# Optimization experiments

Measured on AMD Instinct MI355X. Metric: run time of the kernel, lower is better.

Reference implementation:

```python
import jax, jax.numpy as jnp
import numpy as np

D_MODEL = 1024
N_HEADS = 16
D_HEAD = 64
D_MLP = 4096
EPS = 1e-6


def setup_inputs() -> dict:
    key = jax.random.key(0)
    ks = jax.random.split(key, 12)
    s = lambda fan_in: 1.0 / np.sqrt(fan_in)
    x = jax.random.normal(ks[0], (2, 2048, D_MODEL), dtype=jnp.float32)
    inp = {
        "x": x,
        "ln1_w": jnp.ones((D_MODEL,), jnp.float32),
        "ln2_w": jnp.ones((D_MODEL,), jnp.float32),
        "Wq": jax.random.normal(ks[1], (D_MODEL, N_HEADS * D_HEAD), jnp.float32) * s(D_MODEL),
        "bq": jnp.zeros((N_HEADS * D_HEAD,), jnp.float32),
        "Wk": jax.random.normal(ks[2], (D_MODEL, N_HEADS * D_HEAD), jnp.float32) * s(D_MODEL),
        "bk": jnp.zeros((N_HEADS * D_HEAD,), jnp.float32),
        "Wv": jax.random.normal(ks[3], (D_MODEL, N_HEADS * D_HEAD), jnp.float32) * s(D_MODEL),
        "bv": jnp.zeros((N_HEADS * D_HEAD,), jnp.float32),
        "Wo": jax.random.normal(ks[4], (N_HEADS * D_HEAD, D_MODEL), jnp.float32) * s(N_HEADS * D_HEAD),
        "bo": jnp.zeros((D_MODEL,), jnp.float32),
        "Wup": jax.random.normal(ks[5], (D_MODEL, D_MLP), jnp.float32) * s(D_MODEL),
        "bup": jnp.zeros((D_MLP,), jnp.float32),
        "Wdown": jax.random.normal(ks[6], (D_MLP, D_MODEL), jnp.float32) * s(D_MLP),
        "bdown": jnp.zeros((D_MODEL,), jnp.float32),
    }
    return inp


def _rmsnorm(x, w):
    xf = x.astype(jnp.float32)
    norm = jax.lax.rsqrt(jnp.mean(xf * xf, axis=-1, keepdims=True) + EPS)
    return (x * norm).astype(x.dtype) * w


def _attention(x, Wq, bq, Wk, bk, Wv, bv, Wo, bo):
    B, T, _ = x.shape
    q = (x @ Wq + bq).reshape(B, T, N_HEADS, D_HEAD)
    k = (x @ Wk + bk).reshape(B, T, N_HEADS, D_HEAD)
    v = (x @ Wv + bv).reshape(B, T, N_HEADS, D_HEAD)
    # [B, H, Tq, Tk]
    attn = jnp.einsum("bqhd,bkhd->bhqk", q, k) / jnp.sqrt(jnp.float32(D_HEAD))
    causal = jnp.tril(jnp.ones((T, T), dtype=bool))
    attn = jnp.where(causal, attn, -jnp.inf)
    attn = jax.nn.softmax(attn, axis=-1)
    out = jnp.einsum("bhqk,bkhd->bqhd", attn, v).reshape(B, T, N_HEADS * D_HEAD)
    return out @ Wo + bo


def reference(x, ln1_w, ln2_w, Wq, bq, Wk, bk, Wv, bv, Wo, bo, Wup, bup, Wdown, bdown):
    x = x + _attention(_rmsnorm(x, ln1_w), Wq, bq, Wk, bk, Wv, bv, Wo, bo)
    h = _rmsnorm(x, ln2_w)
    mlp = jax.nn.gelu(h @ Wup + bup, approximate=False) @ Wdown + bdown
    return x + mlp
```

## Files before the change

kernel.cpp:

```cpp
#include <hip/hip_runtime.h>
#include <cmath>

#define DM   1024
#define HDS  16
#define DH   64
#define DMLP 4096
#define TSEQ 2048
#define NROW 4096

typedef short bf16x8 __attribute__((ext_vector_type(8)));
typedef float f32x4 __attribute__((ext_vector_type(4)));

__device__ __forceinline__ unsigned short f2bf(float f) {
  union { float f; unsigned u; } v; v.f = f;
  unsigned r = v.u + 0x7fffu + ((v.u >> 16) & 1u);
  return (unsigned short)(r >> 16);
}

__device__ __forceinline__ void gload_lds16(const void* g, void* l) {
  __builtin_amdgcn_global_load_lds(
      (const __attribute__((address_space(1))) unsigned int*)g,
      (__attribute__((address_space(3))) unsigned int*)l, 16, 0, 0);
}

__global__ __launch_bounds__(256) void tr_kernel(const float* __restrict__ in,
                                                 unsigned short* __restrict__ out,
                                                 int K, int N) {
  __shared__ unsigned short tile[32][33];
  int n0 = blockIdx.x * 32, k0 = blockIdx.y * 32;
  int tx = threadIdx.x & 31, ty = threadIdx.x >> 5;
#pragma unroll
  for (int j = 0; j < 4; ++j) {
    int k = ty + j * 8;
    tile[k][tx] = f2bf(in[(size_t)(k0 + k) * N + n0 + tx]);
  }
  __syncthreads();
#pragma unroll
  for (int j = 0; j < 4; ++j) {
    int n = ty + j * 8;
    out[(size_t)(n0 + n) * K + k0 + tx] = tile[tx][n];
  }
}

__global__ void concat3_kernel(const float* __restrict__ a, const float* __restrict__ b,
                               const float* __restrict__ c, float* __restrict__ out, int n) {
  int i = blockIdx.x * 256 + threadIdx.x;
  if (i < n) { out[i] = a[i]; out[n + i] = b[i]; out[2 * n + i] = c[i]; }
}

__global__ __launch_bounds__(256) void rmsnorm_kernel(const float* __restrict__ x,
                                                      const float* __restrict__ w,
                                                      unsigned short* __restrict__ out) {
  int row = blockIdx.x;
  int t = threadIdx.x;
  const float4* xr = (const float4*)(x + (size_t)row * DM);
  float4 v = xr[t];
  float ss = v.x * v.x + v.y * v.y + v.z * v.z + v.w * v.w;
#pragma unroll
  for (int m = 1; m < 64; m <<= 1) ss += __shfl_xor(ss, m, 64);
  __shared__ float sred[4];
  if ((t & 63) == 0) sred[t >> 6] = ss;
  __syncthreads();
  ss = sred[0] + sred[1] + sred[2] + sred[3];
  float norm = rsqrtf(ss * (1.0f / DM) + 1e-6f);
  float4 wv = ((const float4*)w)[t];
  ushort4 o;
  o.x = f2bf(v.x * norm * wv.x);
  o.y = f2bf(v.y * norm * wv.y);
  o.z = f2bf(v.z * norm * wv.z);
  o.w = f2bf(v.w * norm * wv.w);
  ((ushort4*)out)[(size_t)row * (DM / 4) + t] = o;
}

template <int EPI>
__global__ __launch_bounds__(256) void gemm_bt(const unsigned short* __restrict__ A,
                                               const unsigned short* __restrict__ BT,
                                               const float* __restrict__ bias,
                                               const float* __restrict__ res,
                                               void* __restrict__ outp,
                                               int M, int N, int K) {
  __shared__ alignas(16) unsigned short As[2][128 * 32];
  __shared__ alignas(16) unsigned short Bs[2][128 * 32];
  int tid = threadIdx.x;
  int w = tid >> 6, l = tid & 63;
  unsigned nx = gridDim.x;
  unsigned bidl = blockIdx.y * nx + blockIdx.x;
  unsigned nwg = nx * gridDim.y;
  unsigned cpx = nwg >> 3;
  unsigned sb = (bidl & 7) * cpx + (bidl >> 3);
  int m0 = (int)(sb / nx) * 128, n0 = (int)(sb % nx) * 128;
  int wr = w >> 1, wc = w & 1;
  f32x4 acc[4][4];
#pragma unroll
  for (int i = 0; i < 4; ++i)
#pragma unroll
    for (int j = 0; j < 4; ++j)
#pragma unroll
      for (int e = 0; e < 4; ++e) acc[i][j][e] = 0.0f;

  int nk = K >> 5;
  int arow = tid >> 2, aslot = tid & 3;

#define STG128(BUF, KT)                                                            \
  {                                                                                \
    _Pragma("unroll") for (int i = 0; i < 2; ++i) {                                \
      int row = i * 64 + arow;                                                     \
      gload_lds16(A + (size_t)(m0 + row) * K + (size_t)(KT) * 32 + aslot * 8,      \
                  (char*)As[BUF] + i * 4096 + w * 1024);                           \
      gload_lds16(BT + (size_t)(n0 + row) * K + (size_t)(KT) * 32 + aslot * 8,     \
                  (char*)Bs[BUF] + i * 4096 + w * 1024);                           \
    }                                                                              \
  }

  STG128(0, 0);
  __syncthreads();
  int cur = 0;
  for (int kt = 0; kt < nk; ++kt) {
    if (kt + 1 < nk) STG128(cur ^ 1, kt + 1);
    bf16x8 af[4], bfr[4];
#pragma unroll
    for (int mt = 0; mt < 4; ++mt)
      af[mt] = *(const bf16x8*)((const char*)As[cur] +
                (size_t)(wr * 64 + mt * 16 + (l & 15)) * 64 + (l >> 4) * 16);
#pragma unroll
    for (int nt = 0; nt < 4; ++nt)
      bfr[nt] = *(const bf16x8*)((const char*)Bs[cur] +
                 (size_t)(wc * 64 + nt * 16 + (l & 15)) * 64 + (l >> 4) * 16);
#pragma unroll
    for (int mt = 0; mt < 4; ++mt)
#pragma unroll
      for (int nt = 0; nt < 4; ++nt)
        acc[mt][nt] = __builtin_amdgcn_mfma_f32_16x16x32_bf16(af[mt], bfr[nt], acc[mt][nt], 0, 0, 0);
    __syncthreads();
    cur ^= 1;
  }
#undef STG128

  int g = l >> 4, c = l & 15;
#pragma unroll
  for (int mt = 0; mt < 4; ++mt) {
#pragma unroll
    for (int nt = 0; nt < 4; ++nt) {
#pragma unroll
      for (int r = 0; r < 4; ++r) {
        int m = m0 + wr * 64 + mt * 16 + g * 4 + r;
        int n = n0 + wc * 64 + nt * 16 + c;
        float v = acc[mt][nt][r] + bias[n];
        if (EPI == 2) v = 0.5f * v * (1.0f + erff(v * 0.70710678118654752f));
        if (EPI == 1) {
          v += res[(size_t)m * N + n];
          ((float*)outp)[(size_t)m * N + n] = v;
        } else {
          ((unsigned short*)outp)[(size_t)m * N + n] = f2bf(v);
        }
      }
    }
  }
}

template <int EPI>
__global__ __launch_bounds__(512) void gemm_db256(const unsigned short* __restrict__ A,
                                                  const unsigned short* __restrict__ BT,
                                                  const float* __restrict__ bias,
                                                  const float* __restrict__ res,
                                                  void* __restrict__ outp,
                                                  int M, int N, int K) {
  __shared__ alignas(16) unsigned short As[2][256 * 64];
  __shared__ alignas(16) unsigned short Bs[2][256 * 64];
  int tid = threadIdx.x;
  int w = tid >> 6, l = tid & 63;
  int wr = w >> 2, wc = w & 3;
  unsigned nx = gridDim.x;
  unsigned bidl = blockIdx.y * nx + blockIdx.x;
  unsigned nwg = nx * gridDim.y;
  unsigned cpx = nwg >> 3;
  unsigned sb = (bidl & 7) * cpx + (bidl >> 3);
  int m0 = (int)(sb / nx) * 256, n0 = (int)(sb % nx) * 256;

  f32x4 acc[8][4];
#pragma unroll
  for (int i = 0; i < 8; ++i)
#pragma unroll
    for (int j = 0; j < 4; ++j)
#pragma unroll
      for (int e = 0; e < 4; ++e) acc[i][j][e] = 0.0f;

  int nk = K >> 6;
  int srow = tid >> 3, sslot = tid & 7;
  int gslot = sslot ^ (srow & 7);
  int c = l & 15, g = l >> 4;

#define STG256(BUF, KT)                                                            \
  {                                                                                \
    _Pragma("unroll") for (int i = 0; i < 4; ++i) {                                \
      int row = i * 64 + srow;                                                     \
      gload_lds16(A + (size_t)(m0 + row) * K + (size_t)(KT) * 64 + gslot * 8,      \
                  (char*)As[BUF] + i * 8192 + w * 1024);                           \
      gload_lds16(BT + (size_t)(n0 + row) * K + (size_t)(KT) * 64 + gslot * 8,     \
                  (char*)Bs[BUF] + i * 8192 + w * 1024);                           \
    }                                                                              \
  }

  STG256(0, 0);
  __syncthreads();
  int cur = 0;
  for (int kt = 0; kt < nk; ++kt) {
    if (kt + 1 < nk) STG256(cur ^ 1, kt + 1);
#pragma unroll
    for (int ks = 0; ks < 2; ++ks) {
      bf16x8 bfr[4];
#pragma unroll
      for (int nt = 0; nt < 4; ++nt) {
        int brow = wc * 64 + nt * 16 + c;
        unsigned bslot = (unsigned)((ks * 4 + g) ^ (brow & 7));
        bfr[nt] = *(const bf16x8*)((const char*)Bs[cur] + (size_t)brow * 128 + bslot * 16);
      }
#pragma unroll
      for (int mt = 0; mt < 8; ++mt) {
        int arow2 = wr * 128 + mt * 16 + c;
        unsigned aslot2 = (unsigned)((ks * 4 + g) ^ (arow2 & 7));
        bf16x8 af = *(const bf16x8*)((const char*)As[cur] + (size_t)arow2 * 128 + aslot2 * 16);
#pragma unroll
        for (int nt = 0; nt < 4; ++nt)
          acc[mt][nt] = __builtin_amdgcn_mfma_f32_16x16x32_bf16(af, bfr[nt], acc[mt][nt], 0, 0, 0);
      }
    }
    __syncthreads();
    cur ^= 1;
  }
#undef STG256

#pragma unroll
  for (int mt = 0; mt < 8; ++mt) {
#pragma unroll
    for (int nt = 0; nt < 4; ++nt) {
#pragma unroll
      for (int r = 0; r < 4; ++r) {
        int m = m0 + wr * 128 + mt * 16 + g * 4 + r;
        int n = n0 + wc * 64 + nt * 16 + c;
        float v = acc[mt][nt][r] + bias[n];
        if (EPI == 2) v = 0.5f * v * (1.0f + erff(v * 0.70710678118654752f));
        if (EPI == 1) {
          v += res[(size_t)m * N + n];
          ((float*)outp)[(size_t)m * N + n] = v;
        } else {
          ((unsigned short*)outp)[(size_t)m * N + n] = f2bf(v);
        }
      }
    }
  }
}

__global__ __launch_bounds__(256) void vtr_kernel(const unsigned short* __restrict__ qkv,
                                                  unsigned short* __restrict__ vt) {
  __shared__ unsigned short tile[64][72];
  int bh = blockIdx.y, t0 = blockIdx.x * 64;
  int b = bh >> 4, h = bh & 15;
  int r = threadIdx.x >> 3, sl = threadIdx.x & 7;
#pragma unroll
  for (int half = 0; half < 2; ++half) {
    int rr = r + half * 32;
    bf16x8 v = *(const bf16x8*)(qkv + (size_t)(b * TSEQ + t0 + rr) * 3072 + 2048 + h * 64 + sl * 8);
    *(bf16x8*)&tile[rr][sl * 8] = v;
  }
  __syncthreads();
#pragma unroll
  for (int half = 0; half < 2; ++half) {
    int d = r + half * 32;
    bf16x8 o;
#pragma unroll
    for (int j = 0; j < 8; ++j) o[j] = (short)tile[sl * 8 + j][d];
    *(bf16x8*)(vt + ((size_t)bh * 64 + d) * TSEQ + t0 + sl * 8) = o;
  }
}

__global__ __launch_bounds__(256) void attn_kernel(const unsigned short* __restrict__ qkv,
                                                   const unsigned short* __restrict__ vt,
                                                   unsigned short* __restrict__ attn_out) {
  __shared__ alignas(16) unsigned short Ks[2][64 * 64];
  __shared__ alignas(16) unsigned short Vs[2][64 * 64];
  __shared__ alignas(16) unsigned short Ps[4][16 * 64];
  int tid = threadIdx.x, w = tid >> 6, l = tid & 63, g = l >> 4, c = l & 15;
  int bid = blockIdx.x;
  int qb = 31 - (bid & 31);
  int bh = bid >> 5, b = bh >> 4, h = bh & 15;
  int q0 = qb * 64;
  int qw = q0 + w * 16;

  bf16x8 qf[2];
#pragma unroll
  for (int s = 0; s < 2; ++s)
    qf[s] = *(const bf16x8*)(qkv + (size_t)(b * TSEQ + qw + c) * 3072 + h * 64 + s * 32 + g * 8);

  f32x4 o[4];
  float mrow[4], lpart[4];
#pragma unroll
  for (int dc = 0; dc < 4; ++dc)
#pragma unroll
    for (int e = 0; e < 4; ++e) o[dc][e] = 0.0f;
#pragma unroll
  for (int r = 0; r < 4; ++r) { mrow[r] = -1e30f; lpart[r] = 0.0f; }

  int ntile = qb + 1;
  int sr = tid >> 3, ss = tid & 7;
  bf16x8 kreg[2], vreg[2];

#define LOADT(K0)                                                                       \
  {                                                                                     \
    _Pragma("unroll") for (int hf = 0; hf < 2; ++hf) {                                  \
      int rr = sr + hf * 32;                                                            \
      kreg[hf] = *(const bf16x8*)(qkv + (size_t)(b * TSEQ + (K0) + rr) * 3072 + 1024 +  \
                                  h * 64 + ss * 8);                                     \
      vreg[hf] = *(const bf16x8*)(vt + ((size_t)bh * 64 + rr) * TSEQ + (K0) + ss * 8);  \
    }                                                                                   \
  }
#define WRITET(BUF)                                                                     \
  {                                                                                     \
    _Pragma("unroll") for (int hf = 0; hf < 2; ++hf) {                                  \
      int rr = sr + hf * 32;                                                            \
      unsigned off = (unsigned)(rr * 128 + ss * 16) ^ (unsigned)((rr & 7) << 4);        \
      *(bf16x8*)((char*)Ks[BUF] + off) = kreg[hf];                                      \
      *(bf16x8*)((char*)Vs[BUF] + off) = vreg[hf];                                      \
    }                                                                                   \
  }

  LOADT(0);
  WRITET(0);
  __syncthreads();

  for (int t = 0; t < ntile; ++t) {
    int k0 = t << 6, cur = t & 1;
    if (t + 1 < ntile) LOADT((t + 1) << 6);

    {
      const char* Kb = (const char*)Ks[cur];
      const char* Vb = (const char*)Vs[cur];
      f32x4 s[4];
#pragma unroll
      for (int ni = 0; ni < 4; ++ni) {
        int krow = ni * 16 + c;
        unsigned swz = (unsigned)((c & 7) << 4);
        bf16x8 kf0 = *(const bf16x8*)(Kb + (((unsigned)(krow * 128) + g * 16) ^ swz));
        bf16x8 kf1 = *(const bf16x8*)(Kb + (((unsigned)(krow * 128) + 64 + g * 16) ^ swz));
        f32x4 acc;
#pragma unroll
        for (int e = 0; e < 4; ++e) acc[e] = 0.0f;
        acc = __builtin_amdgcn_mfma_f32_16x16x32_bf16(qf[0], kf0, acc, 0, 0, 0);
        acc = __builtin_amdgcn_mfma_f32_16x16x32_bf16(qf[1], kf1, acc, 0, 0, 0);
        s[ni] = acc;
      }
      bool full = (k0 + 63 <= qw);
#pragma unroll
      for (int r = 0; r < 4; ++r) {
        int qg = qw + g * 4 + r;
        float pm[4];
#pragma unroll
        for (int ni = 0; ni < 4; ++ni) {
          float v = s[ni][r] * 0.125f;
          if (!full) {
            int kg = k0 + ni * 16 + c;
            v = (kg <= qg) ? v : -1e30f;
          }
          pm[ni] = v;
        }
        float mx = fmaxf(fmaxf(pm[0], pm[1]), fmaxf(pm[2], pm[3]));
        mx = fmaxf(mx, __shfl_xor(mx, 1, 64));
        mx = fmaxf(mx, __shfl_xor(mx, 2, 64));
        mx = fmaxf(mx, __shfl_xor(mx, 4, 64));
        mx = fmaxf(mx, __shfl_xor(mx, 8, 64));
        float mnew = fmaxf(mrow[r], mx);
        float scale = __expf(mrow[r] - mnew);
        mrow[r] = mnew;
        float p[4], rs = 0.0f;
#pragma unroll
        for (int ni = 0; ni < 4; ++ni) { p[ni] = __expf(pm[ni] - mnew); rs += p[ni]; }
        lpart[r] = lpart[r] * scale + rs;
#pragma unroll
        for (int dc = 0; dc < 4; ++dc) o[dc][r] *= scale;
        int prow = g * 4 + r;
        unsigned pswz = (unsigned)((prow & 7) << 4);
#pragma unroll
        for (int ni = 0; ni < 4; ++ni)
          *(unsigned short*)((char*)Ps[w] +
                             (((unsigned)(prow * 128 + (ni * 16 + c) * 2)) ^ pswz)) = f2bf(p[ni]);
      }
      asm volatile("s_waitcnt lgkmcnt(0)" ::: "memory");
      unsigned swz = (unsigned)((c & 7) << 4);
#pragma unroll
      for (int kc = 0; kc < 2; ++kc) {
        bf16x8 pf = *(const bf16x8*)((const char*)Ps[w] +
                     (((unsigned)(c * 128 + kc * 64 + g * 16)) ^ swz));
#pragma unroll
        for (int dc = 0; dc < 4; ++dc) {
          bf16x8 vf = *(const bf16x8*)(Vb +
                       (((unsigned)((dc * 16 + c) * 128 + kc * 64 + g * 16)) ^ swz));
          o[dc] = __builtin_amdgcn_mfma_f32_16x16x32_bf16(pf, vf, o[dc], 0, 0, 0);
        }
      }
    }

    if (t + 1 < ntile) {
      WRITET(cur ^ 1);
      __syncthreads();
    }
  }

#pragma unroll
  for (int r = 0; r < 4; ++r) {
    float lr = lpart[r];
    lr += __shfl_xor(lr, 1, 64);
    lr += __shfl_xor(lr, 2, 64);
    lr += __shfl_xor(lr, 4, 64);
    lr += __shfl_xor(lr, 8, 64);
    float inv = 1.0f / lr;
    size_t row = (size_t)b * TSEQ + qw + g * 4 + r;
    unsigned short* op = attn_out + row * 1024 + h * 64 + c;
#pragma unroll
    for (int dc = 0; dc < 4; ++dc) op[dc * 16] = f2bf(o[dc][r] * inv);
  }
#undef LOADT
#undef WRITET
}

extern "C" void kernel_launch(void* const* d_in, const int* in_sizes, int n_in,
                              void* d_out, int out_size, void* d_ws, size_t ws_size,
                              hipStream_t stream) {
  const float* x    = (const float*)d_in[0];
  const float* ln1w = (const float*)d_in[1];
  const float* ln2w = (const float*)d_in[2];
  const float* Wq   = (const float*)d_in[3];
  const float* bq   = (const float*)d_in[4];
  const float* Wk   = (const float*)d_in[5];
  const float* bk   = (const float*)d_in[6];
  const float* Wv   = (const float*)d_in[7];
  const float* bv   = (const float*)d_in[8];
  const float* Wo   = (const float*)d_in[9];
  const float* bo   = (const float*)d_in[10];
  const float* Wup  = (const float*)d_in[11];
  const float* bup  = (const float*)d_in[12];
  const float* Wdn  = (const float*)d_in[13];
  const float* bdn  = (const float*)d_in[14];

  char* ws = (char*)d_ws;
  unsigned short* xn1   = (unsigned short*)(ws + 0);
  unsigned short* vtb   = (unsigned short*)(ws + 0);
  unsigned short* qkv   = (unsigned short*)(ws + (8ull << 20));
  unsigned short* gbuf  = (unsigned short*)(ws + 0);
  unsigned short* attn  = (unsigned short*)(ws + (32ull << 20));
  float*          x2    = (float*)(ws + (40ull << 20));
  unsigned short* h2    = (unsigned short*)(ws + (56ull << 20));
  unsigned short* WqkvT = (unsigned short*)(ws + (64ull << 20));
  unsigned short* WoT   = (unsigned short*)(ws + (70ull << 20));
  unsigned short* WupT  = (unsigned short*)(ws + (72ull << 20));
  unsigned short* WdnT  = (unsigned short*)(ws + (80ull << 20));
  float*          bqkv  = (float*)(ws + (88ull << 20));

  dim3 blk(256);
  dim3 blk512(512);
  tr_kernel<<<dim3(32, 32), blk, 0, stream>>>(Wq, WqkvT, 1024, 1024);
  tr_kernel<<<dim3(32, 32), blk, 0, stream>>>(Wk, WqkvT + 1024 * 1024, 1024, 1024);
  tr_kernel<<<dim3(32, 32), blk, 0, stream>>>(Wv, WqkvT + 2 * 1024 * 1024, 1024, 1024);
  tr_kernel<<<dim3(32, 32), blk, 0, stream>>>(Wo, WoT, 1024, 1024);
  tr_kernel<<<dim3(128, 32), blk, 0, stream>>>(Wup, WupT, 1024, 4096);
  tr_kernel<<<dim3(32, 128), blk, 0, stream>>>(Wdn, WdnT, 4096, 1024);
  concat3_kernel<<<dim3(4), blk, 0, stream>>>(bq, bk, bv, bqkv, 1024);

  rmsnorm_kernel<<<dim3(NROW), blk, 0, stream>>>(x, ln1w, xn1);
  gemm_db256<0><<<dim3(12, 16), blk512, 0, stream>>>(xn1, WqkvT, bqkv, nullptr, qkv, NROW, 3072, 1024);

  vtr_kernel<<<dim3(32, 32), blk, 0, stream>>>(qkv, vtb);
  attn_kernel<<<dim3(1024), blk, 0, stream>>>(qkv, vtb, attn);

  gemm_bt<1><<<dim3(8, 32), blk, 0, stream>>>(attn, WoT, bo, x, x2, NROW, 1024, 1024);

  rmsnorm_kernel<<<dim3(NROW), blk, 0, stream>>>(x2, ln2w, h2);
  gemm_db256<2><<<dim3(16, 16), blk512, 0, stream>>>(h2, WupT, bup, nullptr, gbuf, NROW, 4096, 1024);
  gemm_bt<1><<<dim3(8, 32), blk, 0, stream>>>(gbuf, WdnT, bdn, x2, d_out, NROW, 1024, 4096);
}
```

Measured before the change: 472.7 us.

## Pair causal query blocks per workgroup to balance load and share K/V tiles

Each attention workgroup now handles two query blocks, a high one (31-p) and a low one (p), so every workgroup processes 33 key tiles in total. Each K/V tile loaded into LDS is reused by both query blocks, and the grid drops from 1024 to 512 workgroups. This balances the triangular causal workload and cuts K/V reloads. The cost is twice the accumulator registers per thread, which may lower occupancy, plus fewer workgroups to spread across the CUs.

```diff
diff --git a/kernel.cpp b/kernel.cpp
--- a/kernel.cpp
+++ b/kernel.cpp
@@ -279,29 +279,32 @@
                                                    unsigned short* __restrict__ attn_out) {
   __shared__ alignas(16) unsigned short Ks[2][64 * 64];
   __shared__ alignas(16) unsigned short Vs[2][64 * 64];
-  __shared__ alignas(16) unsigned short Ps[4][16 * 64];
+  __shared__ alignas(16) unsigned short Ps[4][2][16 * 64];
   int tid = threadIdx.x, w = tid >> 6, l = tid & 63, g = l >> 4, c = l & 15;
   int bid = blockIdx.x;
-  int qb = 31 - (bid & 31);
-  int bh = bid >> 5, b = bh >> 4, h = bh & 15;
-  int q0 = qb * 64;
-  int qw = q0 + w * 16;
-
-  bf16x8 qf[2];
-#pragma unroll
-  for (int s = 0; s < 2; ++s)
-    qf[s] = *(const bf16x8*)(qkv + (size_t)(b * TSEQ + qw + c) * 3072 + h * 64 + s * 32 + g * 8);
-
-  f32x4 o[4];
-  float mrow[4], lpart[4];
+  int pair = bid & 15;
+  int bh = bid >> 4, b = bh >> 4, h = bh & 15;
+  int qbh = 31 - pair, qbl = pair;
+  int qwh = qbh * 64 + w * 16;
+  int qwl = qbl * 64 + w * 16;
+
+  bf16x8 qfh[2], qfl[2];
+#pragma unroll
+  for (int s = 0; s < 2; ++s) {
+    qfh[s] = *(const bf16x8*)(qkv + (size_t)(b * TSEQ + qwh + c) * 3072 + h * 64 + s * 32 + g * 8);
+    qfl[s] = *(const bf16x8*)(qkv + (size_t)(b * TSEQ + qwl + c) * 3072 + h * 64 + s * 32 + g * 8);
+  }
+
+  f32x4 oh[4], ol[4];
+  float mh[4], lh[4], ml[4], ll[4];
 #pragma unroll
   for (int dc = 0; dc < 4; ++dc)
 #pragma unroll
-    for (int e = 0; e < 4; ++e) o[dc][e] = 0.0f;
-#pragma unroll
-  for (int r = 0; r < 4; ++r) { mrow[r] = -1e30f; lpart[r] = 0.0f; }
-
-  int ntile = qb + 1;
+    for (int e = 0; e < 4; ++e) { oh[dc][e] = 0.0f; ol[dc][e] = 0.0f; }
+#pragma unroll
+  for (int r = 0; r < 4; ++r) { mh[r] = -1e30f; lh[r] = 0.0f; ml[r] = -1e30f; ll[r] = 0.0f; }
+
+  int ntile = qbh + 1;
   int sr = tid >> 3, ss = tid & 7;
   bf16x8 kreg[2], vreg[2];
 
@@ -323,6 +326,64 @@
       *(bf16x8*)((char*)Vs[BUF] + off) = vreg[hf];                                      \
     }                                                                                   \
   }
+#define COMPQ(QF, O, MR, LP, QW, PSL)                                                   \
+  {                                                                                     \
+    f32x4 s_[4];                                                                        \
+    _Pragma("unroll") for (int ni = 0; ni < 4; ++ni) {                                  \
+      int krow_ = ni * 16 + c;                                                          \
+      unsigned swz_ = (unsigned)((c & 7) << 4);                                         \
+      bf16x8 kf0_ = *(const bf16x8*)(Kb + (((unsigned)(krow_ * 128) + g * 16) ^ swz_)); \
+      bf16x8 kf1_ = *(const bf16x8*)(Kb + (((unsigned)(krow_ * 128) + 64 + g * 16) ^ swz_)); \
+      f32x4 a_;                                                                         \
+      _Pragma("unroll") for (int e = 0; e < 4; ++e) a_[e] = 0.0f;                       \
+      a_ = __builtin_amdgcn_mfma_f32_16x16x32_bf16(QF[0], kf0_, a_, 0, 0, 0);           \
+      a_ = __builtin_amdgcn_mfma_f32_16x16x32_bf16(QF[1], kf1_, a_, 0, 0, 0);           \
+      s_[ni] = a_;                                                                      \
+    }                                                                                   \
+    bool full_ = (k0 + 63 <= (QW));                                                     \
+    _Pragma("unroll") for (int r = 0; r < 4; ++r) {                                     \
+      int qg_ = (QW) + g * 4 + r;                                                       \
+      float pm_[4];                                                                     \
+      _Pragma("unroll") for (int ni = 0; ni < 4; ++ni) {                                \
+        float v_ = s_[ni][r] * 0.125f;                                                  \
+        if (!full_) {                                                                   \
+          int kg_ = k0 + ni * 16 + c;                                                   \
+          v_ = (kg_ <= qg_) ? v_ : -1e30f;                                              \
+        }                                                                               \
+        pm_[ni] = v_;                                                                   \
+      }                                                                                 \
+      float mx_ = fmaxf(fmaxf(pm_[0], pm_[1]), fmaxf(pm_[2], pm_[3]));                  \
+      mx_ = fmaxf(mx_, __shfl_xor(mx_, 1, 64));                                         \
+      mx_ = fmaxf(mx_, __shfl_xor(mx_, 2, 64));                                         \
+      mx_ = fmaxf(mx_, __shfl_xor(mx_, 4, 64));                                         \
+      mx_ = fmaxf(mx_, __shfl_xor(mx_, 8, 64));                                         \
+      float mnew_ = fmaxf(MR[r], mx_);                                                  \
+      float scale_ = __expf(MR[r] - mnew_);                                             \
+      MR[r] = mnew_;                                                                    \
+      float p_[4], rs_ = 0.0f;                                                          \
+      _Pragma("unroll") for (int ni = 0; ni < 4; ++ni) {                                \
+        p_[ni] = __expf(pm_[ni] - mnew_); rs_ += p_[ni];                                \
+      }                                                                                 \
+      LP[r] = LP[r] * scale_ + rs_;                                                     \
+      _Pragma("unroll") for (int dc = 0; dc < 4; ++dc) O[dc][r] *= scale_;              \
+      int prow_ = g * 4 + r;                                                            \
+      unsigned pswz_ = (unsigned)((prow_ & 7) << 4);                                    \
+      _Pragma("unroll") for (int ni = 0; ni < 4; ++ni)                                  \
+        *(unsigned short*)((char*)Ps[w][PSL] +                                          \
+            (((unsigned)(prow_ * 128 + (ni * 16 + c) * 2)) ^ pswz_)) = f2bf(p_[ni]);    \
+    }                                                                                   \
+    asm volatile("s_waitcnt lgkmcnt(0)" ::: "memory");                                  \
+    unsigned swz2_ = (unsigned)((c & 7) << 4);                                          \
+    _Pragma("unroll") for (int kc = 0; kc < 2; ++kc) {                                  \
+      bf16x8 pf_ = *(const bf16x8*)((const char*)Ps[w][PSL] +                           \
+                    (((unsigned)(c * 128 + kc * 64 + g * 16)) ^ swz2_));                \
+      _Pragma("unroll") for (int dc = 0; dc < 4; ++dc) {                                \
+        bf16x8 vf_ = *(const bf16x8*)(Vb +                                              \
+                      (((unsigned)((dc * 16 + c) * 128 + kc * 64 + g * 16)) ^ swz2_));  \
+        O[dc] = __builtin_amdgcn_mfma_f32_16x16x32_bf16(pf_, vf_, O[dc], 0, 0, 0);      \
+      }                                                                                 \
+    }                                                                                   \
+  }
 
   LOADT(0);
   WRITET(0);
@@ -335,68 +396,8 @@
     {
       const char* Kb = (const char*)Ks[cur];
       const char* Vb = (const char*)Vs[cur];
-      f32x4 s[4];
-#pragma unroll
-      for (int ni = 0; ni < 4; ++ni) {
-        int krow = ni * 16 + c;
-        unsigned swz = (unsigned)((c & 7) << 4);
-        bf16x8 kf0 = *(const bf16x8*)(Kb + (((unsigned)(krow * 128) + g * 16) ^ swz));
-        bf16x8 kf1 = *(const bf16x8*)(Kb + (((unsigned)(krow * 128) + 64 + g * 16) ^ swz));
-        f32x4 acc;
-#pragma unroll
-        for (int e = 0; e < 4; ++e) acc[e] = 0.0f;
-        acc = __builtin_amdgcn_mfma_f32_16x16x32_bf16(qf[0], kf0, acc, 0, 0, 0);
-        acc = __builtin_amdgcn_mfma_f32_16x16x32_bf16(qf[1], kf1, acc, 0, 0, 0);
-        s[ni] = acc;
-      }
-      bool full = (k0 + 63 <= qw);
-#pragma unroll
-      for (int r = 0; r < 4; ++r) {
-        int qg = qw + g * 4 + r;
-        float pm[4];
-#pragma unroll
-        for (int ni = 0; ni < 4; ++ni) {
-          float v = s[ni][r] * 0.125f;
-          if (!full) {
-            int kg = k0 + ni * 16 + c;
-            v = (kg <= qg) ? v : -1e30f;
-          }
-          pm[ni] = v;
-        }
-        float mx = fmaxf(fmaxf(pm[0], pm[1]), fmaxf(pm[2], pm[3]));
-        mx = fmaxf(mx, __shfl_xor(mx, 1, 64));
-        mx = fmaxf(mx, __shfl_xor(mx, 2, 64));
-        mx = fmaxf(mx, __shfl_xor(mx, 4, 64));
-        mx = fmaxf(mx, __shfl_xor(mx, 8, 64));
-        float mnew = fmaxf(mrow[r], mx);
-        float scale = __expf(mrow[r] - mnew);
-        mrow[r] = mnew;
-        float p[4], rs = 0.0f;
-#pragma unroll
-        for (int ni = 0; ni < 4; ++ni) { p[ni] = __expf(pm[ni] - mnew); rs += p[ni]; }
-        lpart[r] = lpart[r] * scale + rs;
-#pragma unroll
-        for (int dc = 0; dc < 4; ++dc) o[dc][r] *= scale;
-        int prow = g * 4 + r;
-        unsigned pswz = (unsigned)((prow & 7) << 4);
-#pragma unroll
-        for (int ni = 0; ni < 4; ++ni)
-          *(unsigned short*)((char*)Ps[w] +
-                             (((unsigned)(prow * 128 + (ni * 16 + c) * 2)) ^ pswz)) = f2bf(p[ni]);
-      }
-      asm volatile("s_waitcnt lgkmcnt(0)" ::: "memory");
-      unsigned swz = (unsigned)((c & 7) << 4);
-#pragma unroll
-      for (int kc = 0; kc < 2; ++kc) {
-        bf16x8 pf = *(const bf16x8*)((const char*)Ps[w] +
-                     (((unsigned)(c * 128 + kc * 64 + g * 16)) ^ swz));
-#pragma unroll
-        for (int dc = 0; dc < 4; ++dc) {
-          bf16x8 vf = *(const bf16x8*)(Vb +
-                       (((unsigned)((dc * 16 + c) * 128 + kc * 64 + g * 16)) ^ swz));
-          o[dc] = __builtin_amdgcn_mfma_f32_16x16x32_bf16(pf, vf, o[dc], 0, 0, 0);
-        }
-      }
+      COMPQ(qfh, oh, mh, lh, qwh, 0);
+      if (k0 <= qwl + 15) COMPQ(qfl, ol, ml, ll, qwl, 1);
     }
 
     if (t + 1 < ntile) {
@@ -407,19 +408,29 @@
 
 #pragma unroll
   for (int r = 0; r < 4; ++r) {
-    float lr = lpart[r];
-    lr += __shfl_xor(lr, 1, 64);
-    lr += __shfl_xor(lr, 2, 64);
-    lr += __shfl_xor(lr, 4, 64);
-    lr += __shfl_xor(lr, 8, 64);
-    float inv = 1.0f / lr;
-    size_t row = (size_t)b * TSEQ + qw + g * 4 + r;
-    unsigned short* op = attn_out + row * 1024 + h * 64 + c;
-#pragma unroll
-    for (int dc = 0; dc < 4; ++dc) op[dc * 16] = f2bf(o[dc][r] * inv);
+    float lrh = lh[r], lrl = ll[r];
+    lrh += __shfl_xor(lrh, 1, 64);
+    lrh += __shfl_xor(lrh, 2, 64);
+    lrh += __shfl_xor(lrh, 4, 64);
+    lrh += __shfl_xor(lrh, 8, 64);
+    lrl += __shfl_xor(lrl, 1, 64);
+    lrl += __shfl_xor(lrl, 2, 64);
+    lrl += __shfl_xor(lrl, 4, 64);
+    lrl += __shfl_xor(lrl, 8, 64);
+    float invh = 1.0f / lrh, invl = 1.0f / lrl;
+    size_t rowh = (size_t)b * TSEQ + qwh + g * 4 + r;
+    size_t rowl = (size_t)b * TSEQ + qwl + g * 4 + r;
+    unsigned short* oph = attn_out + rowh * 1024 + h * 64 + c;
+    unsigned short* opl = attn_out + rowl * 1024 + h * 64 + c;
+#pragma unroll
+    for (int dc = 0; dc < 4; ++dc) {
+      oph[dc * 16] = f2bf(oh[dc][r] * invh);
+      opl[dc * 16] = f2bf(ol[dc][r] * invl);
+    }
   }
 #undef LOADT
 #undef WRITET
+#undef COMPQ
 }
 
 extern "C" void kernel_launch(void* const* d_in, const int* in_sizes, int n_in,
@@ -469,7 +480,7 @@
   gemm_db256<0><<<dim3(12, 16), blk512, 0, stream>>>(xn1, WqkvT, bqkv, nullptr, qkv, NROW, 3072, 1024);
 
   vtr_kernel<<<dim3(32, 32), blk, 0, stream>>>(qkv, vtb);
-  attn_kernel<<<dim3(1024), blk, 0, stream>>>(qkv, vtb, attn);
+  attn_kernel<<<dim3(512), blk, 0, stream>>>(qkv, vtb, attn);
 
   gemm_bt<1><<<dim3(8, 32), blk, 0, stream>>>(attn, WoT, bo, x, x2, NROW, 1024, 1024);
 
```

Measured after the change: 418.2 us. 1.13x faster.
